# Optimization experiments

Measured on AMD Instinct MI355X. Metric: run time of the kernel, lower is better.

The kernel has to match this reference:

```python
import jax, jax.numpy as jnp
import numpy as np

DN = ('NCHW', 'OIHW', 'NCHW')

def conv2d(x, w, b):
    y = jax.lax.conv_general_dilated(x, w, window_strides=(1, 1), padding='SAME', dimension_numbers=DN)
    return y + b[None, :, None, None]

def setup_inputs() -> dict:
    key = jax.random.key(0)
    ks = jax.random.split(key, 8)
    C = 256
    Cq = C // 8
    B, H, W = 8, 56, 56
    fan_out_qk = Cq * 9
    fan_out_v = C * 9
    std_qk = np.sqrt(2.0 / fan_out_qk)  # kaiming_normal fan_out, relu
    std_v = np.sqrt(2.0 / fan_out_v)
    return {
        'x': jax.random.normal(ks[0], (B, C, H, W), dtype=jnp.float32),
        'wq': jax.random.normal(ks[1], (Cq, C, 3, 3), dtype=jnp.float32) * std_qk,
        'bq': jnp.zeros((Cq,), dtype=jnp.float32),
        'wk': jax.random.normal(ks[2], (Cq, C, 3, 3), dtype=jnp.float32) * std_qk,
        'bk': jnp.zeros((Cq,), dtype=jnp.float32),
        'wv': jax.random.normal(ks[3], (C, C, 3, 3), dtype=jnp.float32) * std_v,
        'bv': jnp.zeros((C,), dtype=jnp.float32),
        'gamma': jax.random.uniform(ks[4], (1,), dtype=jnp.float32) * 0.1,
    }

def reference(x, wq, bq, wk, bk, wv, bv, gamma):
    B, C, H, W = x.shape
    N = H * W
    q = conv2d(x, wq, bq).reshape(B, -1, N)   # [B, C/8, N]
    k = conv2d(x, wk, bk).reshape(B, -1, N)   # [B, C/8, N]
    v = conv2d(x, wv, bv).reshape(B, C, N)    # [B, C, N]
    # energy[b,i,j] = sum_d q[b,d,i] * k[b,d,j]  (unscaled)
    energy = jnp.einsum('bdi,bdj->bij', q, k)
    attention = jax.nn.softmax(energy, axis=-1)  # [B, N, N]
    # out[b,c,i] = sum_j v[b,c,j] * attention[b,i,j]
    out = jnp.einsum('bcj,bij->bci', v, attention).reshape(B, C, H, W)
    return gamma[0] * out + x
```

## Files before the change

kernel.cpp:

```cpp
#include <hip/hip_runtime.h>
#include <math.h>

#define B_ 8
#define C_ 256
#define H_ 56
#define W_ 56
#define N_ 3136
#define BN_ (B_*N_)
#define LOG2E 1.44269504088896340736f

typedef __attribute__((ext_vector_type(8))) short short8;
typedef __attribute__((ext_vector_type(4))) float f32x4;
typedef __attribute__((ext_vector_type(16))) float f32x16;
typedef __attribute__((ext_vector_type(4))) unsigned short u16x4;
#define MFMA16(A, Bf, Cf) __builtin_amdgcn_mfma_f32_16x16x32_bf16((A), (Bf), (Cf), 0, 0, 0)
#define MFMA32(A, Bf, Cf) __builtin_amdgcn_mfma_f32_32x32x16_bf16((A), (Bf), (Cf), 0, 0, 0)

#define XT_ELEMS (B_*58*64*256)
#define A_ELEMS  (320*2304)
#define AHI_OFF  (2*XT_ELEMS)
#define ALO_OFF  (AHI_OFF + A_ELEMS)
#define QKT_HI_OFF (ALO_OFF + A_ELEMS)
#define QKT_ELEMS  (B_*N_*64)
#define QKT_LO_OFF (QKT_HI_OFF + QKT_ELEMS)
#define VBF_OFF    (QKT_LO_OFF + QKT_ELEMS)
#define VBF_ELEMS  (B_*C_*N_)

#define QF_ELEMS (B_*196*64*8)


#define SWZ(r, col, c8) ((((r)*64 + (col))*4) + ((c8) ^ ((col) & 3)))

#define PSTR 76
#define VSTR 58

__device__ inline unsigned short f2bf(float f) {
    unsigned u = __float_as_uint(f);
    unsigned r = (u + 0x7fffu + ((u >> 16) & 1u)) >> 16;
    return (unsigned short)r;
}
__device__ inline float bf2f(unsigned short h) {
    return __uint_as_float(((unsigned)h) << 16);
}
__device__ inline float exp2_hw(float x) {
    float r; asm("v_exp_f32 %0, %1" : "=v"(r) : "v"(x)); return r;
}
__device__ inline unsigned cvt_pk_bf16(float lo, float hi) {
    unsigned r; asm("v_cvt_pk_bf16_f32 %0, %1, %2" : "=v"(r) : "v"(lo), "v"(hi)); return r;
}

__global__ __launch_bounds__(256) void zero_pads(
    unsigned short* __restrict__ xhi, unsigned short* __restrict__ xlo)
{
    const int g = blockIdx.x*256 + threadIdx.x;
    const int half = 61440;
    unsigned short* base = (g < half) ? xhi : xlo;
    const int i = (g < half) ? g : g - half;
    const int b = i / 7680, rem = i - b*7680;
    const int slot = rem >> 5, c8 = rem & 31;
    int row, col;
    if (slot < 64)       { row = 0;  col = slot; }
    else if (slot < 128) { row = 57; col = slot - 64; }
    else if (slot < 184) { row = slot - 127; col = 0; }
    else                 { row = slot - 183; col = 57; }
    const size_t o = ((size_t)((b*58 + row)*64 + col))*256 + c8*8;
    *(uint4*)(base + o) = make_uint4(0, 0, 0, 0);
}

__global__ __launch_bounds__(256) void prep_x(
    const float* __restrict__ x,
    unsigned short* __restrict__ xhi, unsigned short* __restrict__ xlo)
{
    __shared__ float xs[64][57];
    const int cc = blockIdx.x, y = blockIdx.y, b = blockIdx.z;
    const int t = threadIdx.x;
    const int c0 = cc * 64;
    for (int idx = t; idx < 64 * 56; idx += 256) {
        const int ch = idx / 56, xc = idx - ch * 56;
        xs[ch][xc] = x[((size_t)(b*C_ + c0 + ch)*H_ + y)*W_ + xc];
    }
    __syncthreads();
    for (int idx = t; idx < 56 * 32; idx += 256) {
        const int xc = idx >> 5, chp = idx & 31;
        const float v0 = xs[2*chp][xc], v1 = xs[2*chp + 1][xc];
        const unsigned short h0 = f2bf(v0), h1 = f2bf(v1);
        const unsigned short l0 = f2bf(v0 - bf2f(h0));
        const unsigned short l1 = f2bf(v1 - bf2f(h1));
        const size_t o = ((size_t)(b*58 + y + 1) * 64 + (xc + 1)) * 256 + c0 + 2*chp;
        *(unsigned*)(xhi + o) = (unsigned)h0 | ((unsigned)h1 << 16);
        *(unsigned*)(xlo + o) = (unsigned)l0 | ((unsigned)l1 << 16);
    }
}

__global__ __launch_bounds__(256) void prep_w(
    const float* __restrict__ wq, const float* __restrict__ wk,
    const float* __restrict__ wv,
    unsigned short* __restrict__ Ahi, unsigned short* __restrict__ Alo)
{
    const int g = blockIdx.x * 256 + threadIdx.x;
    if (g >= 320 * 2304) return;
    const int m = g / 2304, k = g - m * 2304;
    const int s = k >> 8, c = k & 255;
    float w;
    if (m < 32)      w = wq[((size_t)m*C_ + c)*9 + s];
    else if (m < 64) w = wk[((size_t)(m-32)*C_ + c)*9 + s];
    else             w = wv[((size_t)(m-64)*C_ + c)*9 + s];
    const unsigned short h = f2bf(w);
    const int cc = (k >> 5) & 7, quad = (k >> 3) & 3, e = k & 7;
    const size_t o = ((((size_t)(m >> 4)*9 + s)*8 + cc)*64 + (quad*16 + (m & 15)))*8 + e;
    Ahi[o] = h;
    Alo[o] = f2bf(w - bf2f(h));
}

__global__ __launch_bounds__(256) void conv_fused(
    const unsigned short* __restrict__ xhi, const unsigned short* __restrict__ xlo,
    const unsigned short* __restrict__ Ahi, const unsigned short* __restrict__ Alo,
    const float* __restrict__ bq, const float* __restrict__ bk,
    const float* __restrict__ bv,
    unsigned short* __restrict__ qkt_hi, unsigned short* __restrict__ qkt_lo,
    unsigned short* __restrict__ vbf)
{
    __shared__ uint4 SMEM[1552];
    uint4* sH = SMEM;
    uint4* sL = SMEM + 776;
    const int b = blockIdx.x, y = blockIdx.y, z = blockIdx.z;
    const int t = threadIdx.x;
    const int w = t >> 6, L = t & 63;
    const int ln = L & 15, quad = L >> 4;

    if (z == 0) {
        f32x4 acc[4];
#pragma unroll
        for (int nt = 0; nt < 4; nt++) acc[nt] = (f32x4)0.0f;

        uint4 ph[3], pl[3];
#pragma unroll
        for (int i = 0; i < 3; i++) {
            const int idx = t + i*256;
            const int r = idx >> 8, col = (idx >> 2) & 63, c8 = idx & 3;
            const size_t go = ((size_t)((b*58 + y + r)*64 + col))*256 + c8*8;
            ph[i] = *(const uint4*)(xhi + go);
            pl[i] = *(const uint4*)(xlo + go);
        }

        for (int cc = 0; cc < 8; cc++) {
            __syncthreads();
#pragma unroll
            for (int i = 0; i < 3; i++) {
                const int idx = t + i*256;
                const int r = idx >> 8, col = (idx >> 2) & 63, c8 = idx & 3;
                sH[SWZ(r, col, c8)] = ph[i];
                sL[SWZ(r, col, c8)] = pl[i];
            }
            __syncthreads();
            if (cc < 7) {
#pragma unroll
                for (int i = 0; i < 3; i++) {
                    const int idx = t + i*256;
                    const int r = idx >> 8, col = (idx >> 2) & 63, c8 = idx & 3;
                    const size_t go = ((size_t)((b*58 + y + r)*64 + col))*256 + (cc+1)*32 + c8*8;
                    ph[i] = *(const uint4*)(xhi + go);
                    pl[i] = *(const uint4*)(xlo + go);
                }
            }
#pragma unroll
            for (int s = 0; s < 9; s++) {
                const int dx = s % 3 - 1;
                const int r = s / 3;
                const size_t aoff = (((size_t)(w*9 + s)*8 + cc)*64 + L)*8;
                const short8 ah = *(const short8*)(Ahi + aoff);
                const short8 al = *(const short8*)(Alo + aoff);
#pragma unroll
                for (int nt = 0; nt < 4; nt++) {
                    const int col = nt*16 + ln + dx + 1;
                    const int i4 = SWZ(r, col, quad);
                    const short8 bh = *(const short8*)&sH[i4];
                    const short8 bl = *(const short8*)&sL[i4];
                    acc[nt] = MFMA16(ah, bh, acc[nt]);
                    acc[nt] = MFMA16(ah, bl, acc[nt]);
                    acc[nt] = MFMA16(al, bh, acc[nt]);
                }
            }
        }

#pragma unroll
        for (int nt = 0; nt < 4; nt++) {
            const int px = nt*16 + ln;
            if (px >= 56) continue;
            const int pix = y*56 + px;
            u16x4 hi4, lo4;
#pragma unroll
            for (int r = 0; r < 4; r++) {
                const int m = w*16 + quad*4 + r;
                const float bias = (m < 32) ? bq[m] : bk[m - 32];
                float val = acc[nt][r] + bias;
                if (w < 2) val *= LOG2E;
                const unsigned short h = f2bf(val);
                hi4[r] = h;
                lo4[r] = f2bf(val - bf2f(h));
            }
            const int m0 = w*16 + quad*4;
            size_t o;
            if (w < 2) {
                o = ((size_t)(b*196 + (pix >> 4))*64 + (m0 >> 3)*16 + (pix & 15))*8 + (m0 & 7);
            } else {
                const int mk0 = m0 - 32;
                o = (size_t)QF_ELEMS +
                    (((size_t)(b*49 + (pix >> 6))*4 + ((pix >> 4) & 3))*64
                     + (mk0 >> 3)*16 + (pix & 15))*8 + (mk0 & 7);
            }
            *(u16x4*)(qkt_hi + o) = hi4;
            *(u16x4*)(qkt_lo + o) = lo4;
        }
    } else {
        const int mg = z - 1;

        f32x4 acc[2][4];
#pragma unroll
        for (int g2 = 0; g2 < 2; g2++)
#pragma unroll
            for (int nt = 0; nt < 4; nt++) acc[g2][nt] = (f32x4)0.0f;

        uint4 ph[3];
#pragma unroll
        for (int i = 0; i < 3; i++) {
            const int idx = t + i*256;
            const int r = idx >> 8, col = (idx >> 2) & 63, c8 = idx & 3;
            const size_t go = ((size_t)((b*58 + y + r)*64 + col))*256 + c8*8;
            ph[i] = *(const uint4*)(xhi + go);
        }

        for (int cc = 0; cc < 8; cc++) {
            __syncthreads();
#pragma unroll
            for (int i = 0; i < 3; i++) {
                const int idx = t + i*256;
                const int r = idx >> 8, col = (idx >> 2) & 63, c8 = idx & 3;
                sH[SWZ(r, col, c8)] = ph[i];
            }
            __syncthreads();
            if (cc < 7) {
#pragma unroll
                for (int i = 0; i < 3; i++) {
                    const int idx = t + i*256;
                    const int r = idx >> 8, col = (idx >> 2) & 63, c8 = idx & 3;
                    const size_t go = ((size_t)((b*58 + y + r)*64 + col))*256 + (cc+1)*32 + c8*8;
                    ph[i] = *(const uint4*)(xhi + go);
                }
            }
#pragma unroll
            for (int s = 0; s < 9; s++) {
                const int dx = s % 3 - 1;
                const int r = s / 3;
                const size_t a0off = (((size_t)((4 + mg*8 + w*2)*9 + s)*8 + cc)*64 + L)*8;
                const short8 a0 = *(const short8*)(Ahi + a0off);
                const short8 a1 = *(const short8*)(Ahi + a0off + 9*8*64*8);
#pragma unroll
                for (int nt = 0; nt < 4; nt++) {
                    const int col = nt*16 + ln + dx + 1;
                    const short8 bf = *(const short8*)&sH[SWZ(r, col, quad)];
                    acc[0][nt] = MFMA16(a0, bf, acc[0][nt]);
                    acc[1][nt] = MFMA16(a1, bf, acc[1][nt]);
                }
            }
        }

        __syncthreads();
        unsigned short* Vs = (unsigned short*)SMEM;
#pragma unroll
        for (int g2 = 0; g2 < 2; g2++)
#pragma unroll
            for (int nt = 0; nt < 4; nt++) {
                const int px = nt*16 + ln;
                if (px >= 56) continue;
#pragma unroll
                for (int r = 0; r < 4; r++) {
                    const int cl = (w*2 + g2)*16 + quad*4 + r;
                    Vs[cl*VSTR + px] = f2bf(acc[g2][nt][r] + bv[mg*128 + cl]);
                }
            }
        __syncthreads();
        const int p0 = y*56;
        const int hh = L >> 5;
        const int cg = mg*4 + w;
        const int gend = (p0 + 55) >> 4;
        for (int gi = p0 >> 4; gi <= gend; gi++) {
            const int pxl0 = gi*16 + hh*8 - p0;
            if (pxl0 >= 0 && pxl0 + 8 <= 56) {
                const short8 vv = *(const short8*)&Vs[(w*32 + (L & 31))*VSTR + pxl0];
                const size_t o = ((((size_t)(b*8 + cg)*49 + (gi >> 2))*4 + (gi & 3))*64 + L)*8;
                *(short8*)(vbf + o) = vv;
            }
        }
    }
}

__global__ __launch_bounds__(128, 4) void attn_flash2w(
    const unsigned short* __restrict__ qkt_hi, const unsigned short* __restrict__ qkt_lo,
    const unsigned short* __restrict__ vbf,
    unsigned short* __restrict__ op0, unsigned short* __restrict__ op1,
    float* __restrict__ mlbase)
{
    __shared__ unsigned short P[2][32*PSTR];
    __shared__ float alphaL[2][32];

    const int bx = blockIdx.x;
    const int b = bx & 7, it = bx >> 3;
    const int chalf = blockIdx.y;
    const int jh = blockIdx.z;
    const int jt0 = jh * 25, njt = 25 - jh;
    const int i_base = it * 32;
    const int t = threadIdx.x;
    const int w = t >> 6, L = t & 63;
    const int ln = L & 15, quad = L >> 4;
    const int l32 = L & 31, h32 = L >> 5;

    const unsigned short* Kf_hi = qkt_hi + QF_ELEMS;
    const unsigned short* Kf_lo = qkt_lo + QF_ELEMS;

    const size_t qoff = ((size_t)(b*196 + it*2 + w)*64 + L)*8;
    const short8 qh = *(const short8*)(qkt_hi + qoff);
    const short8 ql = *(const short8*)(qkt_lo + qoff);

    float m_run = -INFINITY, l_run = 0.0f;
    f32x16 O0 = (f32x16)0.0f, O1 = (f32x16)0.0f;
    const int cg0 = chalf*4 + w*2;
    const unsigned short* vt0 = vbf + ((size_t)(b*8 + cg0)*49)*2048 + (size_t)L*8;
    const unsigned short* vt1 = vbf + ((size_t)(b*8 + cg0 + 1)*49)*2048 + (size_t)L*8;
    const unsigned short* kbh = Kf_hi + (size_t)b*49*2048 + (size_t)L*8;
    const unsigned short* kbl = Kf_lo + (size_t)b*49*2048 + (size_t)L*8;

    for (int jtl = 0; jtl < njt; jtl++) {
        const int jt = jt0 + jtl;
        const int buf = jtl & 1;

        short8 Va[4], Vb[4];
#pragma unroll
        for (int s = 0; s < 4; s++) {
            Va[s] = *(const short8*)(vt0 + jt*2048 + s*512);
            Vb[s] = *(const short8*)(vt1 + jt*2048 + s*512);
        }

        f32x4 sacc[4];
#pragma unroll
        for (int tj = 0; tj < 4; tj++) {
            const short8 kh = *(const short8*)(kbh + jt*2048 + tj*512);
            const short8 kl = *(const short8*)(kbl + jt*2048 + tj*512);
            f32x4 a = (f32x4)0.0f;
            a = MFMA16(kh, qh, a);
            a = MFMA16(kh, ql, a);
            a = MFMA16(kl, qh, a);
            sacc[tj] = a;
        }
        float mt0 = fmaxf(fmaxf(sacc[0][0], sacc[0][1]), fmaxf(sacc[0][2], sacc[0][3]));
        float mt1 = fmaxf(fmaxf(sacc[1][0], sacc[1][1]), fmaxf(sacc[1][2], sacc[1][3]));
        float mt2 = fmaxf(fmaxf(sacc[2][0], sacc[2][1]), fmaxf(sacc[2][2], sacc[2][3]));
        float mt3 = fmaxf(fmaxf(sacc[3][0], sacc[3][1]), fmaxf(sacc[3][2], sacc[3][3]));
        float mx = fmaxf(fmaxf(mt0, mt1), fmaxf(mt2, mt3));
        mx = fmaxf(mx, __shfl_xor(mx, 16));
        mx = fmaxf(mx, __shfl_xor(mx, 32));

        float alpha = 1.0f;
        if (__any(mx > m_run + 8.0f)) {
            const float m_new = fmaxf(m_run, mx);
            alpha = exp2_hw(m_run - m_new);
            m_run = m_new;
        }

#pragma unroll
        for (int tj = 0; tj < 4; tj++)
#pragma unroll
            for (int r = 0; r < 4; r++)
                sacc[tj][r] = exp2_hw(sacc[tj][r] - m_run);
        float s0 = (sacc[0][0] + sacc[0][1]) + (sacc[0][2] + sacc[0][3]);
        float s1 = (sacc[1][0] + sacc[1][1]) + (sacc[1][2] + sacc[1][3]);
        float s2 = (sacc[2][0] + sacc[2][1]) + (sacc[2][2] + sacc[2][3]);
        float s3 = (sacc[3][0] + sacc[3][1]) + (sacc[3][2] + sacc[3][3]);
        float ps = (s0 + s1) + (s2 + s3);
        ps += __shfl_xor(ps, 16);
        ps += __shfl_xor(ps, 32);
        l_run = l_run * alpha + ps;

        {
            unsigned short* prow = &P[buf][(w*16 + ln)*PSTR];
#pragma unroll
            for (int tj = 0; tj < 4; tj++) {
                uint2 pp;
                pp.x = cvt_pk_bf16(sacc[tj][0], sacc[tj][1]);
                pp.y = cvt_pk_bf16(sacc[tj][2], sacc[tj][3]);
                *(uint2*)(prow + tj*16 + quad*4) = pp;
            }
        }
        if (quad == 0) alphaL[buf][w*16 + ln] = alpha;

        __syncthreads();

        const float a = alphaL[buf][l32];
        if (__any(a != 1.0f)) {
#pragma unroll
            for (int rg = 0; rg < 16; rg++) { O0[rg] *= a; O1[rg] *= a; }
        }
        short8 Bp[4];
#pragma unroll
        for (int s = 0; s < 4; s++) {
            Bp[s] = *(const short8*)&P[buf][l32*PSTR + s*16 + h32*8];
            O0 = MFMA32(Va[s], Bp[s], O0);
        }
#pragma unroll
        for (int s = 0; s < 4; s++)
            O1 = MFMA32(Vb[s], Bp[s], O1);
    }

    if (chalf == 0 && quad == 0) {
        const int i = i_base + w*16 + ln;
        mlbase[jh*BN_ + b*N_ + i]       = m_run;
        mlbase[(2 + jh)*BN_ + b*N_ + i] = l_run;
    }
    unsigned short* OP = jh ? op1 : op0;
    const int pix = i_base + l32;
#pragma unroll
    for (int g = 0; g < 2; g++) {
        const f32x16 Ot = g ? O1 : O0;
        const int cg = chalf*128 + w*64 + g*32;
#pragma unroll
        for (int reg = 0; reg < 16; reg++) {
            const int c = cg + (reg & 3) + 8*(reg >> 2) + 4*h32;
            OP[(size_t)(b*C_ + c)*N_ + pix] = f2bf(Ot[reg]);
        }
    }
}

__global__ __launch_bounds__(256) void coef_pre(
    const float* __restrict__ mlbase, const float* __restrict__ gptr,
    float* __restrict__ coef)
{
    const int i = blockIdx.x*256 + threadIdx.x;
    const float m0 = mlbase[i],        m1 = mlbase[BN_ + i];
    const float l0 = mlbase[2*BN_ + i], l1 = mlbase[3*BN_ + i];
    const float mm = fmaxf(m0, m1);
    const float a0 = exp2_hw(m0 - mm), a1 = exp2_hw(m1 - mm);
    const float inv = gptr[0] / (a0*l0 + a1*l1);
    coef[2*i]   = a0 * inv;
    coef[2*i+1] = a1 * inv;
}

__global__ __launch_bounds__(256) void combine(
    const unsigned short* __restrict__ op0, const unsigned short* __restrict__ op1,
    const float* __restrict__ coef,
    const float* __restrict__ x, float* __restrict__ out)
{
    const int bc = blockIdx.x;
    const int b = bc >> 8;
    const size_t base = (size_t)bc * N_;
    const float2* cf = (const float2*)coef + (size_t)b * N_;
    for (int pq = threadIdx.x; pq < 784; pq += 256) {
        const int p0 = pq * 4;
        const ushort4 o0 = *(const ushort4*)(op0 + base + p0);
        const ushort4 o1 = *(const ushort4*)(op1 + base + p0);
        const float4 xx = *(const float4*)(x + base + p0);
        float4 r;
        {
            const float2 c = cf[p0 + 0];
            r.x = xx.x + c.x*bf2f(o0.x) + c.y*bf2f(o1.x);
        }
        {
            const float2 c = cf[p0 + 1];
            r.y = xx.y + c.x*bf2f(o0.y) + c.y*bf2f(o1.y);
        }
        {
            const float2 c = cf[p0 + 2];
            r.z = xx.z + c.x*bf2f(o0.z) + c.y*bf2f(o1.z);
        }
        {
            const float2 c = cf[p0 + 3];
            r.w = xx.w + c.x*bf2f(o0.w) + c.y*bf2f(o1.w);
        }
        *(float4*)(out + base + p0) = r;
    }
}

extern "C" void kernel_launch(void* const* d_in, const int* in_sizes, int n_in,
                              void* d_out, int out_size, void* d_ws, size_t ws_size,
                              hipStream_t stream)
{
    (void)in_sizes; (void)n_in; (void)out_size; (void)ws_size;
    const float* x  = (const float*)d_in[0];
    const float* wq = (const float*)d_in[1];
    const float* bq = (const float*)d_in[2];
    const float* wk = (const float*)d_in[3];
    const float* bk = (const float*)d_in[4];
    const float* wv = (const float*)d_in[5];
    const float* bv = (const float*)d_in[6];
    const float* gm = (const float*)d_in[7];
    float* out = (float*)d_out;

    unsigned short* u = (unsigned short*)d_ws;
    unsigned short* xhi = u;
    unsigned short* xlo = u + XT_ELEMS;
    unsigned short* Ahi = u + AHI_OFF;
    unsigned short* Alo = u + ALO_OFF;
    unsigned short* qkt_hi = u + QKT_HI_OFF;
    unsigned short* qkt_lo = u + QKT_LO_OFF;
    unsigned short* vbf = u + VBF_OFF;
    float* mlbase = (float*)Ahi;
    float* coef = (float*)Alo;

    hipLaunchKernelGGL(zero_pads, dim3(480), dim3(256), 0, stream, xhi, xlo);
    hipLaunchKernelGGL(prep_x, dim3(4, 56, 8), dim3(256), 0, stream, x, xhi, xlo);
    hipLaunchKernelGGL(prep_w, dim3(2880), dim3(256), 0, stream, wq, wk, wv, Ahi, Alo);
    hipLaunchKernelGGL(conv_fused, dim3(8, 56, 3), dim3(256), 0, stream,
                       xhi, xlo, Ahi, Alo, bq, bk, bv, qkt_hi, qkt_lo, vbf);
    hipLaunchKernelGGL(attn_flash2w, dim3(98*8, 2, 2), dim3(128), 0, stream,
                       qkt_hi, qkt_lo, vbf, xhi, xlo, mlbase);
    hipLaunchKernelGGL(coef_pre, dim3(98), dim3(256), 0, stream, mlbase, gm, coef);
    hipLaunchKernelGGL(combine, dim3(2048), dim3(256), 0, stream,
                       xhi, xlo, coef, x, out);
}
```

Baseline: 324.2 us.

## Double-buffer conv input via direct global-to-LDS loads and merge V blocks

```diff
diff --git a/kernel.cpp b/kernel.cpp
--- a/kernel.cpp
+++ b/kernel.cpp
@@ -29,7 +29,8 @@
 #define QF_ELEMS (B_*196*64*8)
 
 
-#define SWZ(r, col, c8) ((((r)*64 + (col))*4) + ((c8) ^ ((col) & 3)))
+#define SX(col) ((((col) & 3)) ^ (((col) >> 2) & 3))
+#define SWZ(r, col, c8) ((((r)*64 + (col))*4) + ((c8) ^ SX(col)))
 
 #define PSTR 76
 #define VSTR 58
@@ -47,6 +48,12 @@
 }
 __device__ inline unsigned cvt_pk_bf16(float lo, float hi) {
     unsigned r; asm("v_cvt_pk_bf16_f32 %0, %1, %2" : "=v"(r) : "v"(lo), "v"(hi)); return r;
+}
+__device__ inline void gl_lds16(const unsigned short* g, uint4* l) {
+    __builtin_amdgcn_global_load_lds(
+        (const __attribute__((address_space(1))) unsigned int*)g,
+        (__attribute__((address_space(3))) unsigned int*)l,
+        16, 0, 0);
 }
 
 __global__ __launch_bounds__(256) void zero_pads(
@@ -112,7 +119,7 @@
     Alo[o] = f2bf(w - bf2f(h));
 }
 
-__global__ __launch_bounds__(256) void conv_fused(
+__global__ __launch_bounds__(256, 3) void conv_fused(
     const unsigned short* __restrict__ xhi, const unsigned short* __restrict__ xlo,
     const unsigned short* __restrict__ Ahi, const unsigned short* __restrict__ Alo,
     const float* __restrict__ bq, const float* __restrict__ bk,
@@ -120,176 +127,178 @@
     unsigned short* __restrict__ qkt_hi, unsigned short* __restrict__ qkt_lo,
     unsigned short* __restrict__ vbf)
 {
-    __shared__ uint4 SMEM[1552];
-    uint4* sH = SMEM;
-    uint4* sL = SMEM + 776;
+    __shared__ uint4 SMEM[3080];
     const int b = blockIdx.x, y = blockIdx.y, z = blockIdx.z;
     const int t = threadIdx.x;
     const int w = t >> 6, L = t & 63;
     const int ln = L & 15, quad = L >> 4;
 
+    size_t gofs[3];
+#pragma unroll
+    for (int i = 0; i < 3; i++) {
+        const int ci = w*192 + i*64 + L;
+        const int r = ci >> 8, col = (ci >> 2) & 63;
+        const int c8 = (ci & 3) ^ SX(col);
+        gofs[i] = ((size_t)((b*58 + y + r)*64 + col))*256 + c8*8;
+    }
+
     if (z == 0) {
-        f32x4 acc[4];
-#pragma unroll
-        for (int nt = 0; nt < 4; nt++) acc[nt] = (f32x4)0.0f;
-
-        uint4 ph[3], pl[3];
+        const int wrg = w >> 1, wnt = w & 1;
+        f32x4 acc[2][2];
+#pragma unroll
+        for (int i = 0; i < 2; i++) { acc[i][0] = (f32x4)0.0f; acc[i][1] = (f32x4)0.0f; }
+
 #pragma unroll
         for (int i = 0; i < 3; i++) {
-            const int idx = t + i*256;
-            const int r = idx >> 8, col = (idx >> 2) & 63, c8 = idx & 3;
-            const size_t go = ((size_t)((b*58 + y + r)*64 + col))*256 + c8*8;
-            ph[i] = *(const uint4*)(xhi + go);
-            pl[i] = *(const uint4*)(xlo + go);
-        }
+            gl_lds16(xhi + gofs[i], SMEM + w*192 + i*64);
+            gl_lds16(xlo + gofs[i], SMEM + 768 + w*192 + i*64);
+        }
+        __syncthreads();
 
         for (int cc = 0; cc < 8; cc++) {
-            __syncthreads();
-#pragma unroll
-            for (int i = 0; i < 3; i++) {
-                const int idx = t + i*256;
-                const int r = idx >> 8, col = (idx >> 2) & 63, c8 = idx & 3;
-                sH[SWZ(r, col, c8)] = ph[i];
-                sL[SWZ(r, col, c8)] = pl[i];
-            }
-            __syncthreads();
+            const int buf = cc & 1;
+            const uint4* sH = SMEM + buf*1536;
+            const uint4* sL = sH + 768;
             if (cc < 7) {
+                uint4* nB = SMEM + (buf^1)*1536;
 #pragma unroll
                 for (int i = 0; i < 3; i++) {
-                    const int idx = t + i*256;
-                    const int r = idx >> 8, col = (idx >> 2) & 63, c8 = idx & 3;
-                    const size_t go = ((size_t)((b*58 + y + r)*64 + col))*256 + (cc+1)*32 + c8*8;
-                    ph[i] = *(const uint4*)(xhi + go);
-                    pl[i] = *(const uint4*)(xlo + go);
+                    gl_lds16(xhi + gofs[i] + (cc+1)*32, nB + w*192 + i*64);
+                    gl_lds16(xlo + gofs[i] + (cc+1)*32, nB + 768 + w*192 + i*64);
                 }
             }
 #pragma unroll
             for (int s = 0; s < 9; s++) {
                 const int dx = s % 3 - 1;
                 const int r = s / 3;
-                const size_t aoff = (((size_t)(w*9 + s)*8 + cc)*64 + L)*8;
-                const short8 ah = *(const short8*)(Ahi + aoff);
-                const short8 al = *(const short8*)(Alo + aoff);
-#pragma unroll
-                for (int nt = 0; nt < 4; nt++) {
-                    const int col = nt*16 + ln + dx + 1;
+                short8 ah[2], al[2];
+#pragma unroll
+                for (int rgi = 0; rgi < 2; rgi++) {
+                    const int rg = wrg*2 + rgi;
+                    const size_t aoff = (((size_t)(rg*9 + s)*8 + cc)*64 + L)*8;
+                    ah[rgi] = *(const short8*)(Ahi + aoff);
+                    al[rgi] = *(const short8*)(Alo + aoff);
+                }
+#pragma unroll
+                for (int nti = 0; nti < 2; nti++) {
+                    const int col = (wnt*2 + nti)*16 + ln + dx + 1;
                     const int i4 = SWZ(r, col, quad);
                     const short8 bh = *(const short8*)&sH[i4];
                     const short8 bl = *(const short8*)&sL[i4];
-                    acc[nt] = MFMA16(ah, bh, acc[nt]);
-                    acc[nt] = MFMA16(ah, bl, acc[nt]);
-                    acc[nt] = MFMA16(al, bh, acc[nt]);
-                }
-            }
-        }
-
-#pragma unroll
-        for (int nt = 0; nt < 4; nt++) {
-            const int px = nt*16 + ln;
-            if (px >= 56) continue;
-            const int pix = y*56 + px;
-            u16x4 hi4, lo4;
-#pragma unroll
-            for (int r = 0; r < 4; r++) {
-                const int m = w*16 + quad*4 + r;
-                const float bias = (m < 32) ? bq[m] : bk[m - 32];
-                float val = acc[nt][r] + bias;
-                if (w < 2) val *= LOG2E;
-                const unsigned short h = f2bf(val);
-                hi4[r] = h;
-                lo4[r] = f2bf(val - bf2f(h));
-            }
-            const int m0 = w*16 + quad*4;
-            size_t o;
-            if (w < 2) {
-                o = ((size_t)(b*196 + (pix >> 4))*64 + (m0 >> 3)*16 + (pix & 15))*8 + (m0 & 7);
-            } else {
-                const int mk0 = m0 - 32;
-                o = (size_t)QF_ELEMS +
-                    (((size_t)(b*49 + (pix >> 6))*4 + ((pix >> 4) & 3))*64
-                     + (mk0 >> 3)*16 + (pix & 15))*8 + (mk0 & 7);
-            }
-            *(u16x4*)(qkt_hi + o) = hi4;
-            *(u16x4*)(qkt_lo + o) = lo4;
+#pragma unroll
+                    for (int rgi = 0; rgi < 2; rgi++) {
+                        acc[rgi][nti] = MFMA16(ah[rgi], bh, acc[rgi][nti]);
+                        acc[rgi][nti] = MFMA16(ah[rgi], bl, acc[rgi][nti]);
+                        acc[rgi][nti] = MFMA16(al[rgi], bh, acc[rgi][nti]);
+                    }
+                }
+            }
+            if (cc < 7) __syncthreads();
+        }
+
+#pragma unroll
+        for (int rgi = 0; rgi < 2; rgi++) {
+            const int rg = wrg*2 + rgi;
+            const int m0 = rg*16 + quad*4;
+#pragma unroll
+            for (int nti = 0; nti < 2; nti++) {
+                const int px = (wnt*2 + nti)*16 + ln;
+                if (px >= 56) continue;
+                const int pix = y*56 + px;
+                u16x4 hi4, lo4;
+#pragma unroll
+                for (int r = 0; r < 4; r++) {
+                    const int m = m0 + r;
+                    const float bias = (m < 32) ? bq[m] : bk[m - 32];
+                    float val = acc[rgi][nti][r] + bias;
+                    if (rg < 2) val *= LOG2E;
+                    const unsigned short h = f2bf(val);
+                    hi4[r] = h;
+                    lo4[r] = f2bf(val - bf2f(h));
+                }
+                size_t o;
+                if (rg < 2) {
+                    o = ((size_t)(b*196 + (pix >> 4))*64 + (m0 >> 3)*16 + (pix & 15))*8 + (m0 & 7);
+                } else {
+                    const int mk0 = m0 - 32;
+                    o = (size_t)QF_ELEMS +
+                        (((size_t)(b*49 + (pix >> 6))*4 + ((pix >> 4) & 3))*64
+                         + (mk0 >> 3)*16 + (pix & 15))*8 + (mk0 & 7);
+                }
+                *(u16x4*)(qkt_hi + o) = hi4;
+                *(u16x4*)(qkt_lo + o) = lo4;
+            }
         }
     } else {
-        const int mg = z - 1;
-
-        f32x4 acc[2][4];
-#pragma unroll
-        for (int g2 = 0; g2 < 2; g2++)
-#pragma unroll
-            for (int nt = 0; nt < 4; nt++) acc[g2][nt] = (f32x4)0.0f;
-
-        uint4 ph[3];
-#pragma unroll
-        for (int i = 0; i < 3; i++) {
-            const int idx = t + i*256;
-            const int r = idx >> 8, col = (idx >> 2) & 63, c8 = idx & 3;
-            const size_t go = ((size_t)((b*58 + y + r)*64 + col))*256 + c8*8;
-            ph[i] = *(const uint4*)(xhi + go);
-        }
+        f32x4 acc[4][4];
+#pragma unroll
+        for (int rg = 0; rg < 4; rg++)
+#pragma unroll
+            for (int nt = 0; nt < 4; nt++) acc[rg][nt] = (f32x4)0.0f;
+
+#pragma unroll
+        for (int i = 0; i < 3; i++)
+            gl_lds16(xhi + gofs[i], SMEM + w*192 + i*64);
+        __syncthreads();
 
         for (int cc = 0; cc < 8; cc++) {
-            __syncthreads();
-#pragma unroll
-            for (int i = 0; i < 3; i++) {
-                const int idx = t + i*256;
-                const int r = idx >> 8, col = (idx >> 2) & 63, c8 = idx & 3;
-                sH[SWZ(r, col, c8)] = ph[i];
-            }
-            __syncthreads();
+            const int buf = cc & 1;
+            const uint4* sH = SMEM + buf*768;
             if (cc < 7) {
-#pragma unroll
-                for (int i = 0; i < 3; i++) {
-                    const int idx = t + i*256;
-                    const int r = idx >> 8, col = (idx >> 2) & 63, c8 = idx & 3;
-                    const size_t go = ((size_t)((b*58 + y + r)*64 + col))*256 + (cc+1)*32 + c8*8;
-                    ph[i] = *(const uint4*)(xhi + go);
-                }
+                uint4* nB = SMEM + (buf^1)*768;
+#pragma unroll
+                for (int i = 0; i < 3; i++)
+                    gl_lds16(xhi + gofs[i] + (cc+1)*32, nB + w*192 + i*64);
             }
 #pragma unroll
             for (int s = 0; s < 9; s++) {
                 const int dx = s % 3 - 1;
                 const int r = s / 3;
-                const size_t a0off = (((size_t)((4 + mg*8 + w*2)*9 + s)*8 + cc)*64 + L)*8;
-                const short8 a0 = *(const short8*)(Ahi + a0off);
-                const short8 a1 = *(const short8*)(Ahi + a0off + 9*8*64*8);
+                short8 a[4];
+#pragma unroll
+                for (int rg = 0; rg < 4; rg++) {
+                    const size_t aoff = (((size_t)((4 + w*4 + rg)*9 + s)*8 + cc)*64 + L)*8;
+                    a[rg] = *(const short8*)(Ahi + aoff);
+                }
 #pragma unroll
                 for (int nt = 0; nt < 4; nt++) {
                     const int col = nt*16 + ln + dx + 1;
                     const short8 bf = *(const short8*)&sH[SWZ(r, col, quad)];
-                    acc[0][nt] = MFMA16(a0, bf, acc[0][nt]);
-                    acc[1][nt] = MFMA16(a1, bf, acc[1][nt]);
-                }
-            }
-        }
-
-        __syncthreads();
+#pragma unroll
+                    for (int rg = 0; rg < 4; rg++)
+                        acc[rg][nt] = MFMA16(a[rg], bf, acc[rg][nt]);
+                }
+            }
+            __syncthreads();
+        }
+
         unsigned short* Vs = (unsigned short*)SMEM;
 #pragma unroll
-        for (int g2 = 0; g2 < 2; g2++)
+        for (int rg = 0; rg < 4; rg++)
 #pragma unroll
             for (int nt = 0; nt < 4; nt++) {
                 const int px = nt*16 + ln;
                 if (px >= 56) continue;
 #pragma unroll
                 for (int r = 0; r < 4; r++) {
-                    const int cl = (w*2 + g2)*16 + quad*4 + r;
-                    Vs[cl*VSTR + px] = f2bf(acc[g2][nt][r] + bv[mg*128 + cl]);
+                    const int cl = (w*4 + rg)*16 + quad*4 + r;
+                    Vs[cl*VSTR + px] = f2bf(acc[rg][nt][r] + bv[cl]);
                 }
             }
         __syncthreads();
         const int p0 = y*56;
-        const int hh = L >> 5;
-        const int cg = mg*4 + w;
+        const int hh = L >> 5, c31 = L & 31;
         const int gend = (p0 + 55) >> 4;
         for (int gi = p0 >> 4; gi <= gend; gi++) {
             const int pxl0 = gi*16 + hh*8 - p0;
             if (pxl0 >= 0 && pxl0 + 8 <= 56) {
-                const short8 vv = *(const short8*)&Vs[(w*32 + (L & 31))*VSTR + pxl0];
-                const size_t o = ((((size_t)(b*8 + cg)*49 + (gi >> 2))*4 + (gi & 3))*64 + L)*8;
-                *(short8*)(vbf + o) = vv;
+#pragma unroll
+                for (int cgk = 0; cgk < 2; cgk++) {
+                    const int cg = w*2 + cgk;
+                    const short8 vv = *(const short8*)&Vs[(cg*32 + c31)*VSTR + pxl0];
+                    const size_t o = ((((size_t)(b*8 + cg)*49 + (gi >> 2))*4 + (gi & 3))*64 + L)*8;
+                    *(short8*)(vbf + o) = vv;
+                }
             }
         }
     }
@@ -459,22 +468,10 @@
         const ushort4 o1 = *(const ushort4*)(op1 + base + p0);
         const float4 xx = *(const float4*)(x + base + p0);
         float4 r;
-        {
-            const float2 c = cf[p0 + 0];
-            r.x = xx.x + c.x*bf2f(o0.x) + c.y*bf2f(o1.x);
-        }
-        {
-            const float2 c = cf[p0 + 1];
-            r.y = xx.y + c.x*bf2f(o0.y) + c.y*bf2f(o1.y);
-        }
-        {
-            const float2 c = cf[p0 + 2];
-            r.z = xx.z + c.x*bf2f(o0.z) + c.y*bf2f(o1.z);
-        }
-        {
-            const float2 c = cf[p0 + 3];
-            r.w = xx.w + c.x*bf2f(o0.w) + c.y*bf2f(o1.w);
-        }
+        { const float2 c = cf[p0 + 0]; r.x = xx.x + c.x*bf2f(o0.x) + c.y*bf2f(o1.x); }
+        { const float2 c = cf[p0 + 1]; r.y = xx.y + c.x*bf2f(o0.y) + c.y*bf2f(o1.y); }
+        { const float2 c = cf[p0 + 2]; r.z = xx.z + c.x*bf2f(o0.z) + c.y*bf2f(o1.z); }
+        { const float2 c = cf[p0 + 3]; r.w = xx.w + c.x*bf2f(o0.w) + c.y*bf2f(o1.w); }
         *(float4*)(out + base + p0) = r;
     }
 }
@@ -508,7 +505,7 @@
     hipLaunchKernelGGL(zero_pads, dim3(480), dim3(256), 0, stream, xhi, xlo);
     hipLaunchKernelGGL(prep_x, dim3(4, 56, 8), dim3(256), 0, stream, x, xhi, xlo);
     hipLaunchKernelGGL(prep_w, dim3(2880), dim3(256), 0, stream, wq, wk, wv, Ahi, Alo);
-    hipLaunchKernelGGL(conv_fused, dim3(8, 56, 3), dim3(256), 0, stream,
+    hipLaunchKernelGGL(conv_fused, dim3(8, 56, 2), dim3(256), 0, stream,
                        xhi, xlo, Ahi, Alo, bq, bk, bv, qkt_hi, qkt_lo, vbf);
     hipLaunchKernelGGL(attn_flash2w, dim3(98*8, 2, 2), dim3(128), 0, stream,
                        qkt_hi, qkt_lo, vbf, xhi, xlo, mlbase);
```

Measured after the change: 307.0 us. 5.3% less time.
